# Performance work log

Measured on AMD Instinct MI355X. Metric: run time of the kernel, lower is better.

The kernel has to match this reference:

```python
import jax, jax.numpy as jnp
import numpy as np

TWO_PI = 6.283185307179586


def setup_inputs() -> dict:
    key = jax.random.key(0)
    k1, k2, k3, k4, k5, k6 = jax.random.split(key, 6)
    B, T, D = 2, 8192, 1024
    x = jax.random.normal(k1, (B, T, D), dtype=jnp.float32)
    # nn.Linear weights are [out, in]; init with small scale like torch default
    s = 1.0 / np.sqrt(D)
    Wk = jax.random.uniform(k2, (D, D), jnp.float32, -s, s)
    Wv = jax.random.uniform(k3, (D, D), jnp.float32, -s, s)
    Wo = jax.random.uniform(k4, (D, D), jnp.float32, -s, s)
    # random phasor frequencies in [0, 2*pi)
    freqs = jax.random.uniform(k5, (D,), jnp.float32, 0.0, TWO_PI)
    return {"x": x, "Wk": Wk, "Wv": Wv, "Wo": Wo, "freqs": freqs}


def reference(x, Wk, Wv, Wo, freqs):
    B, T, C = x.shape
    # k projection is computed in the original forward but never used downstream
    k_real = x @ Wk.T  # [B,T,D] (dead value, kept for fidelity)
    v_real = x @ Wv.T  # [B,T,D]
    v = v_real.astype(jnp.complex64)
    # rotors: per-position unit phasors exp(i * t * freqs), shape [T, D]
    t = jnp.arange(T, dtype=jnp.float32)
    rotors = jnp.exp(1j * (t[:, None] * freqs[None, :])).astype(jnp.complex64)
    # bind each value with its rotor and accumulate causally (O(N) memory trace)
    memory_trace = jnp.cumsum(v * rotors[None, :, :], axis=1)  # [B,T,D] complex64
    # retrieve by unbinding with the conjugate rotor; take the real component
    retrieved = jnp.real(memory_trace * jnp.conj(rotors)[None, :, :])  # [B,T,D]
    return retrieved @ Wo.T
```

## Files before the change

kernel.cpp:

```cpp
#include <hip/hip_runtime.h>
#include <hip/hip_bf16.h>


#define B_  2
#define T_  8192
#define D_  1024
#define BT_ 16384
#define CS_ 32
#define NCHUNK_ 256

typedef __attribute__((ext_vector_type(4))) float f32x4;
typedef __attribute__((ext_vector_type(8))) short bf16x8;
typedef __attribute__((ext_vector_type(8))) unsigned short ushort8;

static __device__ inline unsigned short f2bf(float f) {
    union { float f; unsigned int u; } a;
    a.f = f;
    unsigned int u = a.u;
    return (unsigned short)((u + 0x7FFFu + ((u >> 16) & 1u)) >> 16);
}
static __device__ inline float bf2f(unsigned short h) {
    union { unsigned int u; float f; } a;
    a.u = ((unsigned int)h) << 16;
    return a.f;
}

__global__ __launch_bounds__(256) void cast_all(const float* __restrict__ x,
                                                const float* __restrict__ Wv,
                                                const float* __restrict__ Wo,
                                                unsigned short* __restrict__ xb,
                                                unsigned short* __restrict__ wvb,
                                                unsigned short* __restrict__ wob) {
    const int nx = BT_ * D_ / 8;
    const int nw = D_ * D_ / 8;
    int i = blockIdx.x * 256 + threadIdx.x;
    const float4* src;
    unsigned short* dst;
    int j;
    if (i < nx)            { src = (const float4*)x;  dst = xb;  j = i; }
    else if (i < nx + nw)  { src = (const float4*)Wv; dst = wvb; j = i - nx; }
    else                   { src = (const float4*)Wo; dst = wob; j = i - nx - nw; }
    float4 a = src[j * 2];
    float4 b = src[j * 2 + 1];
    ushort8 o;
    o[0] = f2bf(a.x); o[1] = f2bf(a.y); o[2] = f2bf(a.z); o[3] = f2bf(a.w);
    o[4] = f2bf(b.x); o[5] = f2bf(b.y); o[6] = f2bf(b.z); o[7] = f2bf(b.w);
    *(ushort8*)&dst[(size_t)j * 8] = o;
}

template <bool BF16OUT, bool FUSE_SUMS>
__global__ __launch_bounds__(512, 2) void gemm_bt(const short* __restrict__ A,
                                                  const short* __restrict__ Bm,
                                                  void* __restrict__ Cout,
                                                  const float* __restrict__ freqs,
                                                  float* __restrict__ csum,
                                                  int M, int N, int K) {
    __shared__ short lds[65536];
    const int tid = threadIdx.x;
    const int lane = tid & 63;
    const int wave = tid >> 6;
    const int wm = wave >> 2, wn = wave & 3;

    const int nb = N >> 8;
    const int id = blockIdx.x;
    const int xcd = id & 7;
    const int slot = id >> 3;
    const int bn = (slot % nb) * 256;
    const int bm = (xcd * ((M >> 8) >> 3) + slot / nb) * 256;

    const int srow = lane >> 3;
    const int sg = lane & 7;
    const size_t cstep = (size_t)64 * K;
    const short* gA = A + (size_t)(bm + wave * 8 + srow) * K + ((sg ^ srow) * 8);
    const short* gB = Bm + (size_t)(bn + wave * 8 + srow) * K + ((sg ^ srow) * 8);

    auto stage1 = [&](int kt, int g) {
        const int c = g & 3;
        const short* src = ((g & 4) ? gB : gA) + c * cstep + kt * 64;
        short* dst = &lds[(kt & 1) * 32768 + ((g & 4) ? 16384 : 0) + c * 4096 + wave * 512];
        __builtin_amdgcn_global_load_lds(
            (const __attribute__((address_space(1))) void*)src,
            (__attribute__((address_space(3))) void*)dst, 16, 0, 0);
    };

    const int l15 = lane & 15;
    const int c4r = lane >> 4;
    const int swz0 = ((c4r) ^ (lane & 7)) * 8;
    const int swz1 = ((4 + c4r) ^ (lane & 7)) * 8;
    const int abase = (wm * 128 + l15) * 64;
    const int bbase = 16384 + (wn * 64 + l15) * 64;

    f32x4 acc[8][4] = {};

    stage1(0, 0); stage1(0, 1); stage1(0, 2); stage1(0, 3);
    stage1(0, 4); stage1(0, 5); stage1(0, 6); stage1(0, 7);
    stage1(1, 0); stage1(1, 2);
    stage1(1, 4); stage1(1, 5); stage1(1, 6); stage1(1, 7);
    asm volatile("s_waitcnt vmcnt(6)" ::: "memory");
    __builtin_amdgcn_sched_barrier(0);
    __builtin_amdgcn_s_barrier();

    const int NT = K >> 6;
#pragma unroll 1
    for (int t = 0; t < NT; ++t) {
        const int sb = (t & 1) * 32768;
        const bool pf = (t + 2 < NT);
        bf16x8 av[4][2], b01[2][2], b23[2][2];

#pragma unroll
        for (int ii = 0; ii < 4; ++ii) {
            av[ii][0] = *(const bf16x8*)&lds[sb + abase + ii * 1024 + swz0];
            av[ii][1] = *(const bf16x8*)&lds[sb + abase + ii * 1024 + swz1];
        }
#pragma unroll
        for (int j = 0; j < 2; ++j) {
            b01[j][0] = *(const bf16x8*)&lds[sb + bbase + j * 1024 + swz0];
            b01[j][1] = *(const bf16x8*)&lds[sb + bbase + j * 1024 + swz1];
        }
        if (t + 1 < NT) { stage1(t + 1, 1); stage1(t + 1, 3); }
        __builtin_amdgcn_s_barrier();
        asm volatile("s_waitcnt lgkmcnt(0)" ::: "memory");
        __builtin_amdgcn_sched_barrier(0);
        __builtin_amdgcn_s_setprio(1);
#pragma unroll
        for (int ks = 0; ks < 2; ++ks)
#pragma unroll
            for (int ii = 0; ii < 4; ++ii)
#pragma unroll
                for (int j = 0; j < 2; ++j)
                    acc[ii][j] = __builtin_amdgcn_mfma_f32_16x16x32_bf16(
                        av[ii][ks], b01[j][ks], acc[ii][j], 0, 0, 0);
        __builtin_amdgcn_s_setprio(0);
        __builtin_amdgcn_s_barrier();

#pragma unroll
        for (int j = 0; j < 2; ++j) {
            b23[j][0] = *(const bf16x8*)&lds[sb + bbase + (2 + j) * 1024 + swz0];
            b23[j][1] = *(const bf16x8*)&lds[sb + bbase + (2 + j) * 1024 + swz1];
        }
        if (pf) { stage1(t + 2, 0); stage1(t + 2, 2); }
        __builtin_amdgcn_s_barrier();
        asm volatile("s_waitcnt lgkmcnt(0)" ::: "memory");
        __builtin_amdgcn_sched_barrier(0);
        __builtin_amdgcn_s_setprio(1);
#pragma unroll
        for (int ks = 0; ks < 2; ++ks)
#pragma unroll
            for (int ii = 0; ii < 4; ++ii)
#pragma unroll
                for (int j = 0; j < 2; ++j)
                    acc[ii][2 + j] = __builtin_amdgcn_mfma_f32_16x16x32_bf16(
                        av[ii][ks], b23[j][ks], acc[ii][2 + j], 0, 0, 0);
        __builtin_amdgcn_s_setprio(0);
        __builtin_amdgcn_s_barrier();

#pragma unroll
        for (int ii = 0; ii < 4; ++ii) {
            av[ii][0] = *(const bf16x8*)&lds[sb + abase + (4 + ii) * 1024 + swz0];
            av[ii][1] = *(const bf16x8*)&lds[sb + abase + (4 + ii) * 1024 + swz1];
        }
        if (pf) { stage1(t + 2, 4); stage1(t + 2, 5); }
        __builtin_amdgcn_s_barrier();
        asm volatile("s_waitcnt lgkmcnt(0)" ::: "memory");
        __builtin_amdgcn_sched_barrier(0);
        __builtin_amdgcn_s_setprio(1);
#pragma unroll
        for (int ks = 0; ks < 2; ++ks)
#pragma unroll
            for (int ii = 0; ii < 4; ++ii)
#pragma unroll
                for (int j = 0; j < 2; ++j)
                    acc[4 + ii][2 + j] = __builtin_amdgcn_mfma_f32_16x16x32_bf16(
                        av[ii][ks], b23[j][ks], acc[4 + ii][2 + j], 0, 0, 0);
        __builtin_amdgcn_s_setprio(0);
        __builtin_amdgcn_s_barrier();

        if (pf) { stage1(t + 2, 6); stage1(t + 2, 7); }
        if (pf) asm volatile("s_waitcnt vmcnt(8)" ::: "memory");
        else    asm volatile("s_waitcnt vmcnt(0)" ::: "memory");
        __builtin_amdgcn_sched_barrier(0);
        __builtin_amdgcn_s_barrier();
        __builtin_amdgcn_s_setprio(1);
#pragma unroll
        for (int ks = 0; ks < 2; ++ks)
#pragma unroll
            for (int ii = 0; ii < 4; ++ii)
#pragma unroll
                for (int j = 0; j < 2; ++j)
                    acc[4 + ii][j] = __builtin_amdgcn_mfma_f32_16x16x32_bf16(
                        av[ii][ks], b01[j][ks], acc[4 + ii][j], 0, 0, 0);
        __builtin_amdgcn_s_setprio(0);
        __builtin_amdgcn_s_barrier();
    }

    const int row0 = c4r * 4;
#pragma unroll
    for (int i = 0; i < 8; ++i) {
#pragma unroll
        for (int j = 0; j < 4; ++j) {
            const int col = bn + wn * 64 + j * 16 + (lane & 15);
#pragma unroll
            for (int r = 0; r < 4; ++r) {
                const size_t row = (size_t)bm + wm * 128 + i * 16 + row0 + r;
                if constexpr (BF16OUT)
                    ((unsigned short*)Cout)[row * N + col] = f2bf(acc[i][j][r]);
                else
                    ((float*)Cout)[row * N + col] = acc[i][j][r];
            }
        }
    }

    if constexpr (FUSE_SUMS) {
        const int b = bm >> 13;
        const int trow = bm & 8191;
#pragma unroll
        for (int ig2 = 0; ig2 < 4; ++ig2) {
            const int chunk = (trow >> 5) + wm * 4 + ig2;
            const int t0 = trow + wm * 128 + ig2 * 32 + c4r * 4;
#pragma unroll
            for (int j = 0; j < 4; ++j) {
                const int d = bn + wn * 64 + j * 16 + (lane & 15);
                const float f = freqs[d];
                float ss, cc2;
                sincosf((float)t0 * f, &ss, &cc2);
                float s1, c1;
                sincosf(f, &s1, &c1);
                float c2 = c1 * c1 - s1 * s1, s2 = 2.f * c1 * s1;
                float c4 = c2 * c2 - s2 * s2, s4 = 2.f * c2 * s2;
                float c8 = c4 * c4 - s4 * s4, s8 = 2.f * c4 * s4;
                float c12 = c8 * c4 - s8 * s4, s12 = s8 * c4 + c8 * s4;
                float c13 = c12 * c1 - s12 * s1, s13 = s12 * c1 + c12 * s1;
                float ar = 0.f, ai = 0.f;
                float cr = cc2, sr2 = ss;
#pragma unroll
                for (int f2 = 0; f2 < 2; ++f2) {
                    const int i = ig2 * 2 + f2;
#pragma unroll
                    for (int r = 0; r < 4; ++r) {
                        const float w = acc[i][j][r];
                        ar = fmaf(w, cr, ar); ai = fmaf(w, sr2, ai);
                        const float ec = (r < 3) ? c1 : c13;
                        const float es = (r < 3) ? s1 : s13;
                        const float nc = cr * ec - sr2 * es;
                        const float ns = sr2 * ec + cr * es;
                        cr = nc; sr2 = ns;
                    }
                }
                ar += __shfl_xor(ar, 16); ai += __shfl_xor(ai, 16);
                ar += __shfl_xor(ar, 32); ai += __shfl_xor(ai, 32);
                if (c4r == 0)
                    *(float2*)(csum + (((size_t)b * NCHUNK_ + chunk) * D_ + d) * 2) =
                        make_float2(ar, ai);
            }
        }
    }
}

__global__ __launch_bounds__(512) void scan_pass2(float* __restrict__ csum) {
    const int wid = (blockIdx.x * 512 + threadIdx.x) >> 6;
    const int lane = threadIdx.x & 63;
    const int b = wid / D_;
    const int d = wid % D_;
    float2* cs = (float2*)csum;
    const size_t base = (size_t)b * NCHUNK_ * D_ + d;

    float2 s[4];
#pragma unroll
    for (int k = 0; k < 4; ++k)
        s[k] = cs[base + (size_t)(lane * 4 + k) * D_];
    float lr = s[0].x + s[1].x + s[2].x + s[3].x;
    float li = s[0].y + s[1].y + s[2].y + s[3].y;

    float ir = lr, ii = li;
#pragma unroll
    for (int off = 1; off < 64; off <<= 1) {
        float tr = __shfl_up(ir, off);
        float ti = __shfl_up(ii, off);
        if (lane >= off) { ir += tr; ii += ti; }
    }
    float er = ir - lr, ei = ii - li;
#pragma unroll
    for (int k = 0; k < 4; ++k) {
        const float rr = s[k].x, rim = s[k].y;
        cs[base + (size_t)(lane * 4 + k) * D_] = make_float2(er, ei);
        er += rr; ei += rim;
    }
}

__global__ __launch_bounds__(256) void scan_pass3(const unsigned short* __restrict__ v,
                                                  const float* __restrict__ freqs,
                                                  const float* __restrict__ csum,
                                                  unsigned short* __restrict__ ret) {
    const int chunk = blockIdx.x;
    const int d0 = threadIdx.x * 4;
    const int b = blockIdx.z;

    float fr[4], s[4], c[4], sf[4], cf[4], ar[4], ai[4];
    {
        float4 f4 = *(const float4*)(freqs + d0);
        fr[0] = f4.x; fr[1] = f4.y; fr[2] = f4.z; fr[3] = f4.w;
    }
    const float t0f = (float)(chunk * CS_);
#pragma unroll
    for (int k = 0; k < 4; ++k) {
        sincosf(t0f * fr[k], &s[k], &c[k]);
        sincosf(fr[k], &sf[k], &cf[k]);
    }
    {
        const size_t cb = (((size_t)b * NCHUNK_ + chunk) * D_ + d0) * 2;
        const float4 o0 = *(const float4*)(csum + cb);
        const float4 o1 = *(const float4*)(csum + cb + 4);
        ar[0] = o0.x; ai[0] = o0.y; ar[1] = o0.z; ai[1] = o0.w;
        ar[2] = o1.x; ai[2] = o1.y; ar[3] = o1.z; ai[3] = o1.w;
    }
    const uint2* vp = (const uint2*)(v + ((size_t)b * T_ + chunk * CS_) * D_ + d0);
    uint2* rp = (uint2*)(ret + ((size_t)b * T_ + chunk * CS_) * D_ + d0);
    for (int tb = 0; tb < CS_; tb += 8) {
        uint2 w[8];
#pragma unroll
        for (int u = 0; u < 8; ++u) w[u] = vp[(size_t)(tb + u) * (D_ / 4)];
#pragma unroll
        for (int u = 0; u < 8; ++u) {
            float wv[4], o[4];
            wv[0] = bf2f((unsigned short)w[u].x);
            wv[1] = bf2f((unsigned short)(w[u].x >> 16));
            wv[2] = bf2f((unsigned short)w[u].y);
            wv[3] = bf2f((unsigned short)(w[u].y >> 16));
#pragma unroll
            for (int k = 0; k < 4; ++k) {
                ar[k] = fmaf(wv[k], c[k], ar[k]);
                ai[k] = fmaf(wv[k], s[k], ai[k]);
                o[k] = ar[k] * c[k] + ai[k] * s[k];
                float nc = c[k] * cf[k] - s[k] * sf[k];
                float ns = s[k] * cf[k] + c[k] * sf[k];
                c[k] = nc; s[k] = ns;
            }
            uint2 ow;
            ow.x = (unsigned int)f2bf(o[0]) | ((unsigned int)f2bf(o[1]) << 16);
            ow.y = (unsigned int)f2bf(o[2]) | ((unsigned int)f2bf(o[3]) << 16);
            rp[(size_t)(tb + u) * (D_ / 4)] = ow;
        }
    }
}

extern "C" void kernel_launch(void* const* d_in, const int* in_sizes, int n_in,
                              void* d_out, int out_size, void* d_ws, size_t ws_size,
                              hipStream_t stream) {
    const float* x     = (const float*)d_in[0];
    const float* Wv    = (const float*)d_in[2];
    const float* Wo    = (const float*)d_in[3];
    const float* freqs = (const float*)d_in[4];
    float* out = (float*)d_out;

    char* ws = (char*)d_ws;
    unsigned short* x_bf  = (unsigned short*)ws;
    unsigned short* Wv_bf = (unsigned short*)(ws + 33554432);
    unsigned short* Wo_bf = (unsigned short*)(ws + 35651584);
    float*          csum  = (float*)(ws + 37748736);
    unsigned short* ret  = (unsigned short*)ws;
    unsigned short* v_bf = (unsigned short*)d_out;

    cast_all<<<(BT_ * D_ / 8 + 2 * D_ * D_ / 8) / 256, 256, 0, stream>>>(
        x, Wv, Wo, x_bf, Wv_bf, Wo_bf);

    gemm_bt<true, true><<<(BT_ / 256) * (D_ / 256), 512, 0, stream>>>(
        (const short*)x_bf, (const short*)Wv_bf, (void*)v_bf, freqs, csum, BT_, D_, D_);

    scan_pass2<<<(B_ * D_ * 64) / 512, 512, 0, stream>>>(csum);
    dim3 p3grid(NCHUNK_, 1, B_);
    scan_pass3<<<p3grid, 256, 0, stream>>>(v_bf, freqs, csum, ret);

    gemm_bt<false, false><<<(BT_ / 256) * (D_ / 256), 512, 0, stream>>>(
        (const short*)ret, (const short*)Wo_bf, (void*)out, nullptr, nullptr, BT_, D_, D_);
}
```

Baseline: 237.4 us.

## Fuse all stages into one cooperative kernel with grid-wide barriers

Replaces the five separate launches (cast, first GEMM, scan pass 2, scan pass 3, second GEMM) with a single cooperative persistent kernel of 256 blocks. Stages are separated by grid.sync() calls. The aim is to remove per-launch overhead and the gaps between kernels. The cost is that the cast and scan stages now run on a fixed 256-block grid instead of their own launch shapes, and each grid barrier adds its own overhead. The fused kernel also keeps the GEMM's 64K-short shared-memory allocation and launch bounds for every stage.

```diff
diff --git a/kernel.cpp b/kernel.cpp
--- a/kernel.cpp
+++ b/kernel.cpp
@@ -1,5 +1,8 @@
 #include <hip/hip_runtime.h>
 #include <hip/hip_bf16.h>
+#include <hip/hip_cooperative_groups.h>
+
+namespace cg = cooperative_groups;
 
 
 #define B_  2
@@ -25,37 +28,11 @@
     return a.f;
 }
 
-__global__ __launch_bounds__(256) void cast_all(const float* __restrict__ x,
-                                                const float* __restrict__ Wv,
-                                                const float* __restrict__ Wo,
-                                                unsigned short* __restrict__ xb,
-                                                unsigned short* __restrict__ wvb,
-                                                unsigned short* __restrict__ wob) {
-    const int nx = BT_ * D_ / 8;
-    const int nw = D_ * D_ / 8;
-    int i = blockIdx.x * 256 + threadIdx.x;
-    const float4* src;
-    unsigned short* dst;
-    int j;
-    if (i < nx)            { src = (const float4*)x;  dst = xb;  j = i; }
-    else if (i < nx + nw)  { src = (const float4*)Wv; dst = wvb; j = i - nx; }
-    else                   { src = (const float4*)Wo; dst = wob; j = i - nx - nw; }
-    float4 a = src[j * 2];
-    float4 b = src[j * 2 + 1];
-    ushort8 o;
-    o[0] = f2bf(a.x); o[1] = f2bf(a.y); o[2] = f2bf(a.z); o[3] = f2bf(a.w);
-    o[4] = f2bf(b.x); o[5] = f2bf(b.y); o[6] = f2bf(b.z); o[7] = f2bf(b.w);
-    *(ushort8*)&dst[(size_t)j * 8] = o;
-}
-
 template <bool BF16OUT, bool FUSE_SUMS>
-__global__ __launch_bounds__(512, 2) void gemm_bt(const short* __restrict__ A,
-                                                  const short* __restrict__ Bm,
-                                                  void* __restrict__ Cout,
-                                                  const float* __restrict__ freqs,
-                                                  float* __restrict__ csum,
-                                                  int M, int N, int K) {
-    __shared__ short lds[65536];
+__device__ __forceinline__ void gemm_body(const short* A, const short* Bm,
+                                          void* Cout, const float* freqs,
+                                          float* csum, int M, int N, int K,
+                                          short* lds) {
     const int tid = threadIdx.x;
     const int lane = tid & 63;
     const int wave = tid >> 6;
@@ -256,91 +233,130 @@
     }
 }
 
-__global__ __launch_bounds__(512) void scan_pass2(float* __restrict__ csum) {
-    const int wid = (blockIdx.x * 512 + threadIdx.x) >> 6;
-    const int lane = threadIdx.x & 63;
-    const int b = wid / D_;
-    const int d = wid % D_;
-    float2* cs = (float2*)csum;
-    const size_t base = (size_t)b * NCHUNK_ * D_ + d;
-
-    float2 s[4];
-#pragma unroll
-    for (int k = 0; k < 4; ++k)
-        s[k] = cs[base + (size_t)(lane * 4 + k) * D_];
-    float lr = s[0].x + s[1].x + s[2].x + s[3].x;
-    float li = s[0].y + s[1].y + s[2].y + s[3].y;
-
-    float ir = lr, ii = li;
-#pragma unroll
-    for (int off = 1; off < 64; off <<= 1) {
-        float tr = __shfl_up(ir, off);
-        float ti = __shfl_up(ii, off);
-        if (lane >= off) { ir += tr; ii += ti; }
-    }
-    float er = ir - lr, ei = ii - li;
-#pragma unroll
-    for (int k = 0; k < 4; ++k) {
-        const float rr = s[k].x, rim = s[k].y;
-        cs[base + (size_t)(lane * 4 + k) * D_] = make_float2(er, ei);
-        er += rr; ei += rim;
-    }
-}
-
-__global__ __launch_bounds__(256) void scan_pass3(const unsigned short* __restrict__ v,
-                                                  const float* __restrict__ freqs,
-                                                  const float* __restrict__ csum,
-                                                  unsigned short* __restrict__ ret) {
-    const int chunk = blockIdx.x;
-    const int d0 = threadIdx.x * 4;
-    const int b = blockIdx.z;
-
-    float fr[4], s[4], c[4], sf[4], cf[4], ar[4], ai[4];
+__global__ __launch_bounds__(512, 2) void holo_fused(
+    const float* x, const float* Wv, const float* Wo, const float* freqs,
+    unsigned short* xb,
+    unsigned short* wvb, unsigned short* wob,
+    float* csum,
+    unsigned short* vbf,
+    float* out) {
+    __shared__ short lds[65536];
+    const int tid = threadIdx.x;
+    cg::grid_group grid = cg::this_grid();
+
     {
-        float4 f4 = *(const float4*)(freqs + d0);
-        fr[0] = f4.x; fr[1] = f4.y; fr[2] = f4.z; fr[3] = f4.w;
-    }
-    const float t0f = (float)(chunk * CS_);
-#pragma unroll
-    for (int k = 0; k < 4; ++k) {
-        sincosf(t0f * fr[k], &s[k], &c[k]);
-        sincosf(fr[k], &sf[k], &cf[k]);
-    }
+        const int nx = BT_ * D_ / 8;
+        const int nw = D_ * D_ / 8;
+        const int ntot = nx + 2 * nw;
+        for (int i = blockIdx.x * 512 + tid; i < ntot; i += 256 * 512) {
+            const float4* src;
+            unsigned short* dst;
+            int j;
+            if (i < nx)           { src = (const float4*)x;  dst = xb;  j = i; }
+            else if (i < nx + nw) { src = (const float4*)Wv; dst = wvb; j = i - nx; }
+            else                  { src = (const float4*)Wo; dst = wob; j = i - nx - nw; }
+            float4 a = src[j * 2];
+            float4 b = src[j * 2 + 1];
+            ushort8 o;
+            o[0] = f2bf(a.x); o[1] = f2bf(a.y); o[2] = f2bf(a.z); o[3] = f2bf(a.w);
+            o[4] = f2bf(b.x); o[5] = f2bf(b.y); o[6] = f2bf(b.z); o[7] = f2bf(b.w);
+            *(ushort8*)&dst[(size_t)j * 8] = o;
+        }
+    }
+    grid.sync();
+
+    gemm_body<true, true>((const short*)xb, (const short*)wvb, (void*)vbf,
+                          freqs, csum, BT_, D_, D_, lds);
+    grid.sync();
+
     {
-        const size_t cb = (((size_t)b * NCHUNK_ + chunk) * D_ + d0) * 2;
-        const float4 o0 = *(const float4*)(csum + cb);
-        const float4 o1 = *(const float4*)(csum + cb + 4);
-        ar[0] = o0.x; ai[0] = o0.y; ar[1] = o0.z; ai[1] = o0.w;
-        ar[2] = o1.x; ai[2] = o1.y; ar[3] = o1.z; ai[3] = o1.w;
-    }
-    const uint2* vp = (const uint2*)(v + ((size_t)b * T_ + chunk * CS_) * D_ + d0);
-    uint2* rp = (uint2*)(ret + ((size_t)b * T_ + chunk * CS_) * D_ + d0);
-    for (int tb = 0; tb < CS_; tb += 8) {
-        uint2 w[8];
-#pragma unroll
-        for (int u = 0; u < 8; ++u) w[u] = vp[(size_t)(tb + u) * (D_ / 4)];
-#pragma unroll
-        for (int u = 0; u < 8; ++u) {
-            float wv[4], o[4];
-            wv[0] = bf2f((unsigned short)w[u].x);
-            wv[1] = bf2f((unsigned short)(w[u].x >> 16));
-            wv[2] = bf2f((unsigned short)w[u].y);
-            wv[3] = bf2f((unsigned short)(w[u].y >> 16));
-#pragma unroll
-            for (int k = 0; k < 4; ++k) {
-                ar[k] = fmaf(wv[k], c[k], ar[k]);
-                ai[k] = fmaf(wv[k], s[k], ai[k]);
-                o[k] = ar[k] * c[k] + ai[k] * s[k];
-                float nc = c[k] * cf[k] - s[k] * sf[k];
-                float ns = s[k] * cf[k] + c[k] * sf[k];
-                c[k] = nc; s[k] = ns;
+        const int wid = (blockIdx.x << 3) + (tid >> 6);
+        const int lane = tid & 63;
+        const int b = wid / D_;
+        const int d = wid % D_;
+        float2* cs = (float2*)csum;
+        const size_t base = (size_t)b * NCHUNK_ * D_ + d;
+        float2 s[4];
+#pragma unroll
+        for (int k = 0; k < 4; ++k)
+            s[k] = cs[base + (size_t)(lane * 4 + k) * D_];
+        float lr = s[0].x + s[1].x + s[2].x + s[3].x;
+        float li = s[0].y + s[1].y + s[2].y + s[3].y;
+        float ir = lr, ii = li;
+#pragma unroll
+        for (int off = 1; off < 64; off <<= 1) {
+            float tr = __shfl_up(ir, off);
+            float ti = __shfl_up(ii, off);
+            if (lane >= off) { ir += tr; ii += ti; }
+        }
+        float er = ir - lr, ei = ii - li;
+#pragma unroll
+        for (int k = 0; k < 4; ++k) {
+            const float rr = s[k].x, rim = s[k].y;
+            cs[base + (size_t)(lane * 4 + k) * D_] = make_float2(er, ei);
+            er += rr; ei += rim;
+        }
+    }
+    grid.sync();
+
+    {
+        const int unit = blockIdx.x * 2 + (tid >> 8);
+        const int b = unit >> 8;
+        const int chunk = unit & (NCHUNK_ - 1);
+        const int d0 = (tid & 255) * 4;
+        unsigned short* ret = xb;
+
+        float fr[4], s[4], c[4], sf[4], cf[4], ar[4], ai[4];
+        {
+            float4 f4 = *(const float4*)(freqs + d0);
+            fr[0] = f4.x; fr[1] = f4.y; fr[2] = f4.z; fr[3] = f4.w;
+        }
+        const float t0f = (float)(chunk * CS_);
+#pragma unroll
+        for (int k = 0; k < 4; ++k) {
+            sincosf(t0f * fr[k], &s[k], &c[k]);
+            sincosf(fr[k], &sf[k], &cf[k]);
+        }
+        {
+            const size_t cb = (((size_t)b * NCHUNK_ + chunk) * D_ + d0) * 2;
+            const float4 o0 = *(const float4*)(csum + cb);
+            const float4 o1 = *(const float4*)(csum + cb + 4);
+            ar[0] = o0.x; ai[0] = o0.y; ar[1] = o0.z; ai[1] = o0.w;
+            ar[2] = o1.x; ai[2] = o1.y; ar[3] = o1.z; ai[3] = o1.w;
+        }
+        const uint2* vp = (const uint2*)(vbf + ((size_t)b * T_ + chunk * CS_) * D_ + d0);
+        uint2* rp = (uint2*)(ret + ((size_t)b * T_ + chunk * CS_) * D_ + d0);
+        for (int tb = 0; tb < CS_; tb += 8) {
+            uint2 w[8];
+#pragma unroll
+            for (int u = 0; u < 8; ++u) w[u] = vp[(size_t)(tb + u) * (D_ / 4)];
+#pragma unroll
+            for (int u = 0; u < 8; ++u) {
+                float wv[4], o[4];
+                wv[0] = bf2f((unsigned short)w[u].x);
+                wv[1] = bf2f((unsigned short)(w[u].x >> 16));
+                wv[2] = bf2f((unsigned short)w[u].y);
+                wv[3] = bf2f((unsigned short)(w[u].y >> 16));
+#pragma unroll
+                for (int k = 0; k < 4; ++k) {
+                    ar[k] = fmaf(wv[k], c[k], ar[k]);
+                    ai[k] = fmaf(wv[k], s[k], ai[k]);
+                    o[k] = ar[k] * c[k] + ai[k] * s[k];
+                    float nc = c[k] * cf[k] - s[k] * sf[k];
+                    float ns = s[k] * cf[k] + c[k] * sf[k];
+                    c[k] = nc; s[k] = ns;
+                }
+                uint2 ow;
+                ow.x = (unsigned int)f2bf(o[0]) | ((unsigned int)f2bf(o[1]) << 16);
+                ow.y = (unsigned int)f2bf(o[2]) | ((unsigned int)f2bf(o[3]) << 16);
+                rp[(size_t)(tb + u) * (D_ / 4)] = ow;
             }
-            uint2 ow;
-            ow.x = (unsigned int)f2bf(o[0]) | ((unsigned int)f2bf(o[1]) << 16);
-            ow.y = (unsigned int)f2bf(o[2]) | ((unsigned int)f2bf(o[3]) << 16);
-            rp[(size_t)(tb + u) * (D_ / 4)] = ow;
-        }
-    }
+        }
+    }
+    grid.sync();
+
+    gemm_body<false, false>((const short*)xb, (const short*)wob, (void*)out,
+                            nullptr, nullptr, BT_, D_, D_, lds);
 }
 
 extern "C" void kernel_launch(void* const* d_in, const int* in_sizes, int n_in,
@@ -357,19 +373,11 @@
     unsigned short* Wv_bf = (unsigned short*)(ws + 33554432);
     unsigned short* Wo_bf = (unsigned short*)(ws + 35651584);
     float*          csum  = (float*)(ws + 37748736);
-    unsigned short* ret  = (unsigned short*)ws;
-    unsigned short* v_bf = (unsigned short*)d_out;
-
-    cast_all<<<(BT_ * D_ / 8 + 2 * D_ * D_ / 8) / 256, 256, 0, stream>>>(
-        x, Wv, Wo, x_bf, Wv_bf, Wo_bf);
-
-    gemm_bt<true, true><<<(BT_ / 256) * (D_ / 256), 512, 0, stream>>>(
-        (const short*)x_bf, (const short*)Wv_bf, (void*)v_bf, freqs, csum, BT_, D_, D_);
-
-    scan_pass2<<<(B_ * D_ * 64) / 512, 512, 0, stream>>>(csum);
-    dim3 p3grid(NCHUNK_, 1, B_);
-    scan_pass3<<<p3grid, 256, 0, stream>>>(v_bf, freqs, csum, ret);
-
-    gemm_bt<false, false><<<(BT_ / 256) * (D_ / 256), 512, 0, stream>>>(
-        (const short*)ret, (const short*)Wo_bf, (void*)out, nullptr, nullptr, BT_, D_, D_);
-}
+    unsigned short* v_bf  = (unsigned short*)d_out;
+
+    void* args[] = {(void*)&x, (void*)&Wv, (void*)&Wo, (void*)&freqs,
+                    (void*)&x_bf, (void*)&Wv_bf, (void*)&Wo_bf,
+                    (void*)&csum, (void*)&v_bf, (void*)&out};
+    hipLaunchCooperativeKernel((const void*)holo_fused, dim3(256), dim3(512),
+                               args, 0, stream);
+}
```

Measured after the change: 361.5 us. 1.52x slower.
